# Kernel optimization log

Hardware: AMD Instinct MI355X
Metric: run time of the kernel (lower is better)

## Reference

```python
import jax, jax.numpy as jnp
import numpy as np

N, L, HH, WW, E, NH = 8, 300, 96, 96, 256, 8


def setup_inputs() -> dict:
    key = jax.random.key(0)
    ks = jax.random.split(key, 9)
    return {
        "query_row": jax.random.normal(ks[0], (N, L, E), dtype=jnp.float32),
        "query_col": jax.random.normal(ks[1], (N, L, E), dtype=jnp.float32),
        "key_row": jax.random.normal(ks[2], (N, HH, WW, E), dtype=jnp.float32),
        "key_col": jax.random.normal(ks[3], (N, HH, WW, E), dtype=jnp.float32),
        "value": jax.random.normal(ks[4], (N, HH, WW, E), dtype=jnp.float32),
        "in_proj_weight": jax.random.normal(ks[5], (5 * E, E), dtype=jnp.float32) * 0.02,
        "in_proj_bias": jax.random.normal(ks[6], (5 * E,), dtype=jnp.float32) * 0.02,
        "out_proj_weight": jax.random.normal(ks[7], (E, E), dtype=jnp.float32) * 0.02,
        "out_proj_bias": jax.random.normal(ks[8], (E,), dtype=jnp.float32) * 0.02,
        "num_heads": NH,
    }


def reference(query_row, query_col, key_row, key_col, value,
              in_proj_weight, in_proj_bias, out_proj_weight, out_proj_bias,
              num_heads):
    bsz, tgt_len, embed_dim = query_row.shape
    head_dim = embed_dim // num_heads
    scaling = float(head_dim) ** -0.5

    def proj(x, i):
        w = in_proj_weight[i * embed_dim:(i + 1) * embed_dim]
        b = in_proj_bias[i * embed_dim:(i + 1) * embed_dim]
        return x @ w.T + b

    q_row = proj(query_row, 0) * scaling          # (N, L, E)
    q_col = proj(query_col, 1) * scaling          # (N, L, E)
    k_row = proj(key_row, 2).mean(axis=1)         # mean over H -> (N, W, E)
    k_col = proj(key_col, 3).mean(axis=2)         # mean over W -> (N, H, E)
    v = proj(value, 4)                            # (N, H, W, E)

    heads = lambda t: t.reshape(*t.shape[:-1], num_heads, head_dim)
    qr, qc, kr, kc = heads(q_row), heads(q_col), heads(k_row), heads(k_col)
    vh = heads(v)                                 # (N, H, W, nh, hd)

    # additive row/col decomposed scores -> independent softmaxes
    w_row = jax.nn.softmax(jnp.einsum('blnd,bwnd->bnlw', qr, kr), axis=-1)  # (N,nh,L,W)
    w_col = jax.nn.softmax(jnp.einsum('blnd,bhnd->bnlh', qc, kc), axis=-1)  # (N,nh,L,H)

    # contract col weights with value over H, then row weights over W
    tmp = jnp.einsum('bnlh,bhwnd->bnlwd', w_col, vh)       # (N,nh,L,W,hd)
    out = jnp.einsum('bnlw,bnlwd->blnd', w_row, tmp)       # (N,L,nh,hd)
    out = out.reshape(bsz, tgt_len, embed_dim).transpose(1, 0, 2)  # (L,N,E)
    return out @ out_proj_weight.T + out_proj_bias
```

## Files before the change

kernel.cpp:

```cpp
#include <hip/hip_runtime.h>
#include <cstdint>


typedef __attribute__((ext_vector_type(8))) short short8v;
typedef __attribute__((ext_vector_type(4))) short short4v;
typedef __attribute__((ext_vector_type(4))) float f32x4;

#define SCALE_Q 0.17677669529663687f

#define GLL16(gp, lp)                                                   \
  __builtin_amdgcn_global_load_lds(                                     \
      (const __attribute__((address_space(1))) void*)(gp),              \
      (__attribute__((address_space(3))) void*)(lp), 16, 0, 0)

__device__ __forceinline__ unsigned short f2bf(float x) {
  unsigned int u = __builtin_bit_cast(unsigned int, x);
  u += 0x7FFFu + ((u >> 16) & 1u);
  return (unsigned short)(u >> 16);
}

__device__ __forceinline__ unsigned int cvtpk(float a, float b) {
  unsigned int r;
  asm("v_cvt_pk_bf16_f32 %0, %1, %2" : "=v"(r) : "v"(a), "v"(b));
  return r;
}

__device__ __forceinline__ short8v pack8cvt(const f32x4& lo, const f32x4& hi) {
  union { short8v s; unsigned int u[4]; } z;
  z.u[0] = cvtpk(lo[0], lo[1]);
  z.u[1] = cvtpk(lo[2], lo[3]);
  z.u[2] = cvtpk(hi[0], hi[1]);
  z.u[3] = cvtpk(hi[2], hi[3]);
  return z.s;
}

__device__ __forceinline__ short4v pack4cvt(float a, float b, float c, float d) {
  union { short4v s; unsigned int u[2]; } z;
  z.u[0] = cvtpk(a, b);
  z.u[1] = cvtpk(c, d);
  return z.s;
}

__device__ __forceinline__ short8v pack8(const float4& fa, const float4& fb) {
  short8v v;
  v[0] = (short)f2bf(fa.x); v[1] = (short)f2bf(fa.y);
  v[2] = (short)f2bf(fa.z); v[3] = (short)f2bf(fa.w);
  v[4] = (short)f2bf(fb.x); v[5] = (short)f2bf(fb.y);
  v[6] = (short)f2bf(fb.z); v[7] = (short)f2bf(fb.w);
  return v;
}

__global__ __launch_bounds__(256) void cvt_w_kernel(const float* __restrict__ w_in,
                                                    const float* __restrict__ w_out,
                                                    short* __restrict__ Wb) {
  int idx = blockIdx.x * 256 + threadIdx.x;
  float v = (idx < 327680) ? w_in[idx] : w_out[idx - 327680];
  Wb[idx] = (short)f2bf(v);
}

__global__ __launch_bounds__(512, 4) void mega1_kernel(
    const float* __restrict__ A, const short* __restrict__ Wb,
    const float* __restrict__ bias, short* __restrict__ vvT,
    const float* __restrict__ key_row, const float* __restrict__ key_col,
    float* __restrict__ krm, float* __restrict__ kcm) {
  __shared__ float buf[2][16 * 260];
  __shared__ short Ts[8][32 * 36];
  int blk = blockIdx.x;
  int t = threadIdx.x;

  if ((blk & 1) == 0) {
    int vb_id = blk >> 1;
    int wave = t >> 6, lane = t & 63, r = lane & 15, g = lane >> 4;
    int m0g = vb_id * 96;
    int b_ = vb_id / 96;
    int hw00 = (vb_id - b_ * 96) * 96;
    int chbase = wave * 32;

    short8v bf[8][2];
    {
      const short* wbase = Wb + (size_t)(chbase + r) * 256;
#pragma unroll
      for (int ks = 0; ks < 8; ++ks)
#pragma unroll
        for (int nf = 0; nf < 2; ++nf)
          bf[ks][nf] = *(const short8v*)(wbase + nf * 16 * 256 + ks * 32 + g * 8);
    }
#pragma unroll
    for (int ks = 0; ks < 8; ++ks)
#pragma unroll
      for (int nf = 0; nf < 2; ++nf)
        asm volatile("" : "+a"(bf[ks][nf]));
    float bias_v[2];
#pragma unroll
    for (int nf = 0; nf < 2; ++nf) bias_v[nf] = bias[chbase + nf * 16 + r];

#pragma unroll
    for (int q = 0; q < 2; ++q) {
#pragma unroll
      for (int i = 0; i < 2; ++i) {
        int row = wave * 2 + i;
        const float* gp = A + ((size_t)m0g + q * 16 + row) * 256 + lane * 4;
        GLL16(gp, &buf[q][row * 260]);
      }
    }

    int chg = chbase + (lane & 31);
    int half = lane >> 5;
    short* vbase = vvT + (size_t)(b_ * 8 + (chg >> 5)) * 294912 +
                   (size_t)(chg & 31) * 9216 + hw00;
    const short* tsr = &Ts[wave][(lane & 31) * 36];

#pragma unroll
    for (int tt = 0; tt < 6; ++tt) {
      if (tt == 5)                  asm volatile("s_waitcnt vmcnt(0)" ::: "memory");
      else if (tt == 2 || tt == 4)  asm volatile("s_waitcnt vmcnt(4)" ::: "memory");
      else                          asm volatile("s_waitcnt vmcnt(2)" ::: "memory");
      __builtin_amdgcn_s_barrier();

      f32x4 acc[2] = {};
      const float* bp_ = &buf[tt & 1][0];
#pragma unroll
      for (int ks = 0; ks < 8; ++ks) {
        const float* p = bp_ + r * 260 + ks * 32 + g * 8;
        f32x4 lo = *(const f32x4*)p;
        f32x4 hi = *(const f32x4*)(p + 4);
        short8v af = pack8cvt(lo, hi);
        acc[0] = __builtin_amdgcn_mfma_f32_16x16x32_bf16(af, bf[ks][0], acc[0], 0, 0, 0);
        acc[1] = __builtin_amdgcn_mfma_f32_16x16x32_bf16(af, bf[ks][1], acc[1], 0, 0, 0);
      }

#pragma unroll
      for (int nf = 0; nf < 2; ++nf) {
        float bv = bias_v[nf];
        *(short4v*)&Ts[wave][(nf * 16 + r) * 36 + (tt & 1) * 16 + g * 4] =
            pack4cvt(acc[nf][0] + bv, acc[nf][1] + bv, acc[nf][2] + bv, acc[nf][3] + bv);
      }
      asm volatile("" ::: "memory");

      if (tt & 1) {
        short* gdst = vbase + (tt - 1) * 16 + half * 16;
        const short* src = tsr + half * 16;
        *(short8v*)gdst = *(const short8v*)src;
        *(short8v*)(gdst + 8) = *(const short8v*)(src + 8);
        asm volatile("" ::: "memory");
      }

      __builtin_amdgcn_s_barrier();
      if (tt + 2 < 6) {
#pragma unroll
        for (int i = 0; i < 2; ++i) {
          int row = wave * 2 + i;
          const float* gp = A + ((size_t)m0g + (tt + 2) * 16 + row) * 256 + lane * 4;
          GLL16(gp, &buf[tt & 1][row * 260]);
        }
      }
    }
  } else {
    int id = blk >> 1;
    int sub = t >> 8, u = t & 255;
    int e4 = u & 63, q4 = u >> 6;
    float4* part4 = (float4*)&buf[0][0];
    if (id < 384) {
      int bw = id * 2 + sub;
      int b = bw / 96, w = bw - b * 96;
      const float4* p = (const float4*)(key_row + ((size_t)b * 9216 + w) * 256) +
                        e4 + (size_t)q4 * 24 * 6144;
      float4 s = {0.f, 0.f, 0.f, 0.f};
#pragma unroll
      for (int i = 0; i < 24; ++i) {
        float4 v = p[(size_t)i * 6144];
        s.x += v.x; s.y += v.y; s.z += v.z; s.w += v.w;
      }
      part4[sub * 256 + u] = s;
      __syncthreads();
      if (u < 64) {
        float4 a = part4[sub * 256 + u], c = part4[sub * 256 + u + 64];
        float4 d = part4[sub * 256 + u + 128], e = part4[sub * 256 + u + 192];
        float4 o;
        o.x = (a.x + c.x + d.x + e.x) * (1.f / 96.f);
        o.y = (a.y + c.y + d.y + e.y) * (1.f / 96.f);
        o.z = (a.z + c.z + d.z + e.z) * (1.f / 96.f);
        o.w = (a.w + c.w + d.w + e.w) * (1.f / 96.f);
        ((float4*)krm)[(size_t)bw * 64 + u] = o;
      }
    } else {
      int bh = (id - 384) * 2 + sub;
      const float4* p = (const float4*)(key_col + (size_t)bh * 24576) + e4 +
                        (size_t)q4 * 24 * 64;
      float4 s = {0.f, 0.f, 0.f, 0.f};
#pragma unroll
      for (int i = 0; i < 24; ++i) {
        float4 v = p[(size_t)i * 64];
        s.x += v.x; s.y += v.y; s.z += v.z; s.w += v.w;
      }
      part4[sub * 256 + u] = s;
      __syncthreads();
      if (u < 64) {
        float4 a = part4[sub * 256 + u], c = part4[sub * 256 + u + 64];
        float4 d = part4[sub * 256 + u + 128], e = part4[sub * 256 + u + 192];
        float4 o;
        o.x = (a.x + c.x + d.x + e.x) * (1.f / 96.f);
        o.y = (a.y + c.y + d.y + e.y) * (1.f / 96.f);
        o.z = (a.z + c.z + d.z + e.z) * (1.f / 96.f);
        o.w = (a.w + c.w + d.w + e.w) * (1.f / 96.f);
        ((float4*)kcm)[(size_t)bh * 64 + u] = o;
      }
    }
  }
}

__global__ __launch_bounds__(512) void gemm512(
    const float* __restrict__ krm, const float* __restrict__ kcm,
    const float* __restrict__ qrow, const float* __restrict__ qcol,
    const short* __restrict__ Wb, const float* __restrict__ Bv,
    short* __restrict__ krb, short* __restrict__ kcb,
    short* __restrict__ qrb, short* __restrict__ qcb) {
  __shared__ short As[2][32 * 264];
  int id = blockIdx.x;
  const float* A; short* Cb; const short* Wp; const float* bp; int M, m064;
  float scale;
  if (id < 12)      { A = krm;  Cb = krb; Wp = Wb + 131072; bp = Bv + 512; M = 768;  m064 = id * 64;        scale = 1.f; }
  else if (id < 24) { A = kcm;  Cb = kcb; Wp = Wb + 196608; bp = Bv + 768; M = 768;  m064 = (id - 12) * 64; scale = 1.f; }
  else if (id < 62) { A = qrow; Cb = qrb; Wp = Wb;          bp = Bv;       M = 2400; m064 = (id - 24) * 64; scale = SCALE_Q; }
  else              { A = qcol; Cb = qcb; Wp = Wb + 65536;  bp = Bv + 256; M = 2400; m064 = (id - 62) * 64; scale = SCALE_Q; }

  int t = threadIdx.x, sub = t >> 8, u = t & 255;
  int wave = u >> 6, lane = u & 63, r = lane & 15, g = lane >> 4;
  int m0 = m064 + sub * 32;

  {
    int row = u >> 3, c0 = (u & 7) * 32;
    int mrow = m0 + row; if (mrow >= M) mrow = M - 1;
    const float* ap = A + (size_t)mrow * 256 + c0;
    float4 ld[8];
#pragma unroll
    for (int j = 0; j < 8; ++j) ld[j] = *(const float4*)(ap + j * 4);
    short* dst = &As[sub][row * 264 + c0];
#pragma unroll
    for (int j = 0; j < 4; ++j)
      *(short8v*)(dst + j * 8) = pack8(ld[2 * j], ld[2 * j + 1]);
  }
  __syncthreads();

  f32x4 acc[2][4] = {};
  const short* wbase = Wp + (size_t)(wave * 64 + r) * 256;
#pragma unroll
  for (int ks = 0; ks < 8; ++ks) {
    short8v af0 = *(const short8v*)&As[sub][r * 264 + ks * 32 + g * 8];
    short8v af1 = *(const short8v*)&As[sub][(16 + r) * 264 + ks * 32 + g * 8];
    short8v bf[4];
#pragma unroll
    for (int nf = 0; nf < 4; ++nf)
      bf[nf] = *(const short8v*)(wbase + nf * 16 * 256 + ks * 32 + g * 8);
#pragma unroll
    for (int nf = 0; nf < 4; ++nf) {
      acc[0][nf] = __builtin_amdgcn_mfma_f32_16x16x32_bf16(af0, bf[nf], acc[0][nf], 0, 0, 0);
      acc[1][nf] = __builtin_amdgcn_mfma_f32_16x16x32_bf16(af1, bf[nf], acc[1][nf], 0, 0, 0);
    }
  }

#pragma unroll
  for (int mf = 0; mf < 2; ++mf)
#pragma unroll
    for (int nf = 0; nf < 4; ++nf) {
      int nn = wave * 64 + nf * 16 + r;
      float bval = bp[nn];
#pragma unroll
      for (int i = 0; i < 4; ++i) {
        int m = m0 + mf * 16 + g * 4 + i;
        if (m >= M) continue;
        Cb[(size_t)m * 256 + nn] = (short)f2bf((acc[mf][nf][i] + bval) * scale);
      }
    }
}

__global__ __launch_bounds__(512) void gemm512_out(
    const float* __restrict__ A0, const float* __restrict__ Aadd,
    const short* __restrict__ Wp, const float* __restrict__ bp,
    float* __restrict__ Cf) {
  __shared__ short As[2][32 * 264];
  const int M = 2400;
  int t = threadIdx.x, sub = t >> 8, u = t & 255;
  int wave = u >> 6, lane = u & 63, r = lane & 15, g = lane >> 4;
  int m0 = blockIdx.x * 64 + sub * 32;

  {
    int row = u >> 3, c0 = (u & 7) * 32;
    int mrow = m0 + row; if (mrow >= M) mrow = M - 1;
    size_t off = (size_t)mrow * 256 + c0;
    const float* ap = A0 + off;
    const float* aq = Aadd + off;
    float4 ld[8];
#pragma unroll
    for (int j = 0; j < 8; ++j) {
      float4 x = *(const float4*)(ap + j * 4);
      float4 e = *(const float4*)(aq + j * 4);
      x.x += e.x; x.y += e.y; x.z += e.z; x.w += e.w;
      ld[j] = x;
    }
    short* dst = &As[sub][row * 264 + c0];
#pragma unroll
    for (int j = 0; j < 4; ++j)
      *(short8v*)(dst + j * 8) = pack8(ld[2 * j], ld[2 * j + 1]);
  }
  __syncthreads();

  f32x4 acc[2][4] = {};
  const short* wbase = Wp + (size_t)(wave * 64 + r) * 256;
#pragma unroll
  for (int ks = 0; ks < 8; ++ks) {
    short8v af0 = *(const short8v*)&As[sub][r * 264 + ks * 32 + g * 8];
    short8v af1 = *(const short8v*)&As[sub][(16 + r) * 264 + ks * 32 + g * 8];
    short8v bf[4];
#pragma unroll
    for (int nf = 0; nf < 4; ++nf)
      bf[nf] = *(const short8v*)(wbase + nf * 16 * 256 + ks * 32 + g * 8);
#pragma unroll
    for (int nf = 0; nf < 4; ++nf) {
      acc[0][nf] = __builtin_amdgcn_mfma_f32_16x16x32_bf16(af0, bf[nf], acc[0][nf], 0, 0, 0);
      acc[1][nf] = __builtin_amdgcn_mfma_f32_16x16x32_bf16(af1, bf[nf], acc[1][nf], 0, 0, 0);
    }
  }

#pragma unroll
  for (int mf = 0; mf < 2; ++mf)
#pragma unroll
    for (int nf = 0; nf < 4; ++nf) {
      int nn = wave * 64 + nf * 16 + r;
      float bval = bp[nn];
#pragma unroll
      for (int i = 0; i < 4; ++i) {
        int m = m0 + mf * 16 + g * 4 + i;
        if (m >= M) continue;
        int bb = m / 300, ll = m - bb * 300;
        Cf[((size_t)ll * 8 + bb) * 256 + nn] = acc[mf][nf][i] + bval;
      }
    }
}

__global__ __launch_bounds__(64) void scores_softmax_v2(
    const short* __restrict__ qrb, const short* __restrict__ qcb,
    const short* __restrict__ krb, const short* __restrict__ kcb,
    short* __restrict__ wrowB, float* __restrict__ wcolT) {
  int lchunk = blockIdx.x, bn = blockIdx.y, kind = blockIdx.z;
  int b = bn >> 3, n = bn & 7;
  int lane = threadIdx.x;
  int r = lane & 15, g = lane >> 4;
  const short* qb = kind ? qcb : qrb;
  const short* kb = kind ? kcb : krb;
  int l0 = lchunk * 80;

  short8v a[5], bfr[6];
#pragma unroll
  for (int lf = 0; lf < 5; ++lf) {
    int l = l0 + lf * 16 + r;
    if (l > 299) l = 299;
    a[lf] = *(const short8v*)(qb + ((size_t)b * 300 + l) * 256 + n * 32 + g * 8);
  }
#pragma unroll
  for (int f = 0; f < 6; ++f)
    bfr[f] = *(const short8v*)(kb + ((size_t)b * 96 + f * 16 + r) * 256 + n * 32 + g * 8);

  f32x4 c[5][6];
#pragma unroll
  for (int lf = 0; lf < 5; ++lf)
#pragma unroll
    for (int f = 0; f < 6; ++f) {
      f32x4 z = {};
      c[lf][f] = __builtin_amdgcn_mfma_f32_16x16x32_bf16(a[lf], bfr[f], z, 0, 0, 0);
    }

#pragma unroll
  for (int lf = 0; lf < 5; ++lf)
#pragma unroll
    for (int i = 0; i < 4; ++i) {
      float m = c[lf][0][i];
#pragma unroll
      for (int f = 1; f < 6; ++f) m = fmaxf(m, c[lf][f][i]);
#pragma unroll
      for (int mask = 1; mask <= 8; mask <<= 1) m = fmaxf(m, __shfl_xor(m, mask, 64));
      float e[6], s = 0.f;
#pragma unroll
      for (int f = 0; f < 6; ++f) { e[f] = __expf(c[lf][f][i] - m); s += e[f]; }
#pragma unroll
      for (int mask = 1; mask <= 8; mask <<= 1) s += __shfl_xor(s, mask, 64);
      float inv = 1.f / s;
#pragma unroll
      for (int f = 0; f < 6; ++f) c[lf][f][i] = e[f] * inv;
    }

  if (kind == 0) {
#pragma unroll
    for (int lf = 0; lf < 5; ++lf)
#pragma unroll
      for (int i = 0; i < 4; ++i) {
        int l = l0 + lf * 16 + g * 4 + i;
        bool ok = (l < 300);
#pragma unroll
        for (int f = 0; f < 6; ++f) {
          float wv = ok ? c[lf][f][i] : 0.f;
          wrowB[((size_t)bn * 320 + l) * 96 + f * 16 + r] = (short)f2bf(wv);
        }
      }
  } else {
#pragma unroll
    for (int lf = 0; lf < 5; ++lf)
#pragma unroll
      for (int f = 0; f < 6; ++f) {
        int l = l0 + lf * 16 + g * 4;
        f32x4 wv = c[lf][f];
#pragma unroll
        for (int i = 0; i < 4; ++i) if (l + i >= 300) wv[i] = 0.f;
        *(f32x4*)(wcolT + ((size_t)bn * 96 + f * 16 + r) * 320 + l) = wv;
      }
  }
}

__global__ __launch_bounds__(512, 2) void attn_kernel(
    const short* __restrict__ wrowB, const float* __restrict__ wcolT,
    const short* __restrict__ vvT, float* __restrict__ part0,
    float* __restrict__ part1) {
  __shared__ f32x4 cmb[3][2][4][64];
  int i = blockIdx.x;
  int xcd = i & 7, j = i >> 3;
  int grp = j / 10, rem = j - grp * 10;
  int bn = grp * 8 + xcd;
  int lh = rem >> 1, hh2 = rem & 1;
  int b = bn >> 3, n = bn & 7;
  int t = threadIdx.x, wave = t >> 6, lane = t & 63;
  int df = wave & 1, hq = wave >> 1;
  int lbase = lh * 64;
  int r = lane & 15, g = lane >> 4;
  int hbase = hh2 * 48 + hq * 12;

  short8v a[4][3];
  const short* wr = wrowB + (size_t)bn * 320 * 96;
#pragma unroll
  for (int lf = 0; lf < 4; ++lf)
#pragma unroll
    for (int ks = 0; ks < 3; ++ks)
      a[lf][ks] = *(const short8v*)(wr + (lbase + lf * 16 + r) * 96 + ks * 32 + g * 8);

  const short* vb = vvT + (size_t)bn * 294912 + (size_t)(df * 16 + r) * 9216 + hbase * 96;
  const float* wcb = wcolT + ((size_t)bn * 96 + hbase) * 320 + lbase + g * 4;

  f32x4 acc[4] = {};
  short8v b0[3], b1[3];
  f32x4 w0[4], w1[4];
#pragma unroll
  for (int ks = 0; ks < 3; ++ks) b0[ks] = *(const short8v*)(vb + ks * 32 + g * 8);
#pragma unroll
  for (int lf = 0; lf < 4; ++lf) w0[lf] = *(const f32x4*)(wcb + lf * 16);

#pragma unroll
  for (int h2 = 0; h2 < 6; ++h2) {
    int h = h2 * 2;
#pragma unroll
    for (int ks = 0; ks < 3; ++ks) b1[ks] = *(const short8v*)(vb + (h + 1) * 96 + ks * 32 + g * 8);
#pragma unroll
    for (int lf = 0; lf < 4; ++lf) w1[lf] = *(const f32x4*)(wcb + (h + 1) * 320 + lf * 16);
    {
      f32x4 R[4] = {};
#pragma unroll
      for (int ks = 0; ks < 3; ++ks)
#pragma unroll
        for (int lf = 0; lf < 4; ++lf)
          R[lf] = __builtin_amdgcn_mfma_f32_16x16x32_bf16(a[lf][ks], b0[ks], R[lf], 0, 0, 0);
#pragma unroll
      for (int lf = 0; lf < 4; ++lf) acc[lf] += w0[lf] * R[lf];
    }
    if (h2 < 5) {
#pragma unroll
      for (int ks = 0; ks < 3; ++ks) b0[ks] = *(const short8v*)(vb + (h + 2) * 96 + ks * 32 + g * 8);
#pragma unroll
      for (int lf = 0; lf < 4; ++lf) w0[lf] = *(const f32x4*)(wcb + (h + 2) * 320 + lf * 16);
    }
    {
      f32x4 R[4] = {};
#pragma unroll
      for (int ks = 0; ks < 3; ++ks)
#pragma unroll
        for (int lf = 0; lf < 4; ++lf)
          R[lf] = __builtin_amdgcn_mfma_f32_16x16x32_bf16(a[lf][ks], b1[ks], R[lf], 0, 0, 0);
#pragma unroll
      for (int lf = 0; lf < 4; ++lf) acc[lf] += w1[lf] * R[lf];
    }
  }

  if (hq > 0) {
#pragma unroll
    for (int lf = 0; lf < 4; ++lf) cmb[hq - 1][df][lf][lane] = acc[lf];
  }
  __syncthreads();
  if (hq == 0) {
    float* po = hh2 ? part1 : part0;
#pragma unroll
    for (int lf = 0; lf < 4; ++lf) {
      f32x4 o = acc[lf];
#pragma unroll
      for (int q = 0; q < 3; ++q) o += cmb[q][df][lf][lane];
#pragma unroll
      for (int i2 = 0; i2 < 4; ++i2) {
        int l = lbase + lf * 16 + g * 4 + i2;
        if (l < 300)
          po[((size_t)b * 300 + l) * 256 + n * 32 + df * 16 + r] = o[i2];
      }
    }
  }
}

extern "C" void kernel_launch(void* const* d_in, const int* in_sizes, int n_in,
                              void* d_out, int out_size, void* d_ws, size_t ws_size,
                              hipStream_t stream) {
  const float* query_row = (const float*)d_in[0];
  const float* query_col = (const float*)d_in[1];
  const float* key_row   = (const float*)d_in[2];
  const float* key_col   = (const float*)d_in[3];
  const float* value     = (const float*)d_in[4];
  const float* W         = (const float*)d_in[5];
  const float* Bv        = (const float*)d_in[6];
  const float* Wout      = (const float*)d_in[7];
  const float* Bout      = (const float*)d_in[8];

  float* ws = (float*)d_ws;
  float* krm   = ws;
  float* kcm   = krm + 196608;
  float* part0 = kcm + 196608;
  float* part1 = part0 + 614400;
  float* wcolT = part1 + 614400;
  short* qrb   = (short*)(wcolT + 1966080);
  short* qcb   = qrb + 614400;
  short* krb   = qcb + 614400;
  short* kcb   = krb + 196608;
  short* wrowB = kcb + 196608;
  short* vvT   = wrowB + 1966080;
  short* Wb    = vvT + 18874368;

  cvt_w_kernel<<<1536, 256, 0, stream>>>(W, Wout, Wb);
  mega1_kernel<<<1536, 512, 0, stream>>>(value, Wb + 262144, Bv + 1024, vvT,
                                         key_row, key_col, krm, kcm);
  gemm512<<<100, 512, 0, stream>>>(krm, kcm, query_row, query_col, Wb, Bv,
                                   krb, kcb, qrb, qcb);
  scores_softmax_v2<<<dim3(4, 64, 2), 64, 0, stream>>>(qrb, qcb, krb, kcb, wrowB, wcolT);
  attn_kernel<<<640, 512, 0, stream>>>(wrowB, wcolT, vvT, part0, part1);
  gemm512_out<<<38, 512, 0, stream>>>(part0, part1, Wb + 327680, Bout, (float*)d_out);
}
```

Before: 155.4 us.

## Restructure attention to stage V in LDS and fuse mean-pool into value projection blocks

The attention kernel is rewritten to use 256 blocks, each covering a quarter of H for one batch-head. V slices are double-buffered in swizzled LDS through global_load_lds, the column weights are staged once in LDS, and each wave handles 80 rows of L. The output partials go to four buffers that the output GEMM now sums. The value-projection kernel no longer interleaves separate mean-pool blocks; every block projects value and then does one key mean-pool chunk, which halves the grid. This trades more LDS use and fewer blocks (less parallelism) for reuse of V across waves, and it adds extra partial traffic.

Measured after the change: 306.1 us. +97.0%, slower.

```diff
diff --git a/kernel.cpp b/kernel.cpp
--- a/kernel.cpp
+++ b/kernel.cpp
@@ -58,153 +58,149 @@
   Wb[idx] = (short)f2bf(v);
 }
 
-__global__ __launch_bounds__(512, 4) void mega1_kernel(
+__global__ __launch_bounds__(512, 4) void vpm_kernel(
     const float* __restrict__ A, const short* __restrict__ Wb,
     const float* __restrict__ bias, short* __restrict__ vvT,
     const float* __restrict__ key_row, const float* __restrict__ key_col,
     float* __restrict__ krm, float* __restrict__ kcm) {
   __shared__ float buf[2][16 * 260];
   __shared__ short Ts[8][32 * 36];
-  int blk = blockIdx.x;
   int t = threadIdx.x;
-
-  if ((blk & 1) == 0) {
-    int vb_id = blk >> 1;
-    int wave = t >> 6, lane = t & 63, r = lane & 15, g = lane >> 4;
-    int m0g = vb_id * 96;
-    int b_ = vb_id / 96;
-    int hw00 = (vb_id - b_ * 96) * 96;
-    int chbase = wave * 32;
-
-    short8v bf[8][2];
-    {
-      const short* wbase = Wb + (size_t)(chbase + r) * 256;
-#pragma unroll
-      for (int ks = 0; ks < 8; ++ks)
-#pragma unroll
-        for (int nf = 0; nf < 2; ++nf)
-          bf[ks][nf] = *(const short8v*)(wbase + nf * 16 * 256 + ks * 32 + g * 8);
-    }
+  int wave = t >> 6, lane = t & 63, r = lane & 15, g = lane >> 4;
+  int m0g = blockIdx.x * 96;
+  int b_ = blockIdx.x / 96;
+  int hw00 = (blockIdx.x - b_ * 96) * 96;
+  int chbase = wave * 32;
+
+  short8v bf[8][2];
+  {
+    const short* wbase = Wb + (size_t)(chbase + r) * 256;
 #pragma unroll
     for (int ks = 0; ks < 8; ++ks)
 #pragma unroll
       for (int nf = 0; nf < 2; ++nf)
-        asm volatile("" : "+a"(bf[ks][nf]));
-    float bias_v[2];
-#pragma unroll
-    for (int nf = 0; nf < 2; ++nf) bias_v[nf] = bias[chbase + nf * 16 + r];
-
-#pragma unroll
-    for (int q = 0; q < 2; ++q) {
+        bf[ks][nf] = *(const short8v*)(wbase + nf * 16 * 256 + ks * 32 + g * 8);
+  }
+#pragma unroll
+  for (int ks = 0; ks < 8; ++ks)
+#pragma unroll
+    for (int nf = 0; nf < 2; ++nf)
+      asm volatile("" : "+a"(bf[ks][nf]));
+  float bias_v[2];
+#pragma unroll
+  for (int nf = 0; nf < 2; ++nf) bias_v[nf] = bias[chbase + nf * 16 + r];
+
+#pragma unroll
+  for (int q = 0; q < 2; ++q) {
+#pragma unroll
+    for (int i = 0; i < 2; ++i) {
+      int row = wave * 2 + i;
+      const float* gp = A + ((size_t)m0g + q * 16 + row) * 256 + lane * 4;
+      GLL16(gp, &buf[q][row * 260]);
+    }
+  }
+
+  int chg = chbase + (lane & 31);
+  int half = lane >> 5;
+  short* vbase = vvT + (size_t)(b_ * 8 + (chg >> 5)) * 294912 +
+                 (size_t)(chg & 31) * 9216 + hw00;
+  const short* tsr = &Ts[wave][(lane & 31) * 36];
+
+#pragma unroll
+  for (int tt = 0; tt < 6; ++tt) {
+    if (tt == 5)                  asm volatile("s_waitcnt vmcnt(0)" ::: "memory");
+    else if (tt == 2 || tt == 4)  asm volatile("s_waitcnt vmcnt(4)" ::: "memory");
+    else                          asm volatile("s_waitcnt vmcnt(2)" ::: "memory");
+    __builtin_amdgcn_s_barrier();
+
+    f32x4 acc[2] = {};
+    const float* bp_ = &buf[tt & 1][0];
+#pragma unroll
+    for (int ks = 0; ks < 8; ++ks) {
+      const float* p = bp_ + r * 260 + ks * 32 + g * 8;
+      f32x4 lo = *(const f32x4*)p;
+      f32x4 hi = *(const f32x4*)(p + 4);
+      short8v af = pack8cvt(lo, hi);
+      acc[0] = __builtin_amdgcn_mfma_f32_16x16x32_bf16(af, bf[ks][0], acc[0], 0, 0, 0);
+      acc[1] = __builtin_amdgcn_mfma_f32_16x16x32_bf16(af, bf[ks][1], acc[1], 0, 0, 0);
+    }
+
+#pragma unroll
+    for (int nf = 0; nf < 2; ++nf) {
+      float bv = bias_v[nf];
+      *(short4v*)&Ts[wave][(nf * 16 + r) * 36 + (tt & 1) * 16 + g * 4] =
+          pack4cvt(acc[nf][0] + bv, acc[nf][1] + bv, acc[nf][2] + bv, acc[nf][3] + bv);
+    }
+    asm volatile("" ::: "memory");
+
+    if (tt & 1) {
+      short* gdst = vbase + (tt - 1) * 16 + half * 16;
+      const short* src = tsr + half * 16;
+      *(short8v*)gdst = *(const short8v*)src;
+      *(short8v*)(gdst + 8) = *(const short8v*)(src + 8);
+      asm volatile("" ::: "memory");
+    }
+
+    __builtin_amdgcn_s_barrier();
+    if (tt + 2 < 6) {
 #pragma unroll
       for (int i = 0; i < 2; ++i) {
         int row = wave * 2 + i;
-        const float* gp = A + ((size_t)m0g + q * 16 + row) * 256 + lane * 4;
-        GLL16(gp, &buf[q][row * 260]);
+        const float* gp = A + ((size_t)m0g + (tt + 2) * 16 + row) * 256 + lane * 4;
+        GLL16(gp, &buf[tt & 1][row * 260]);
       }
     }
-
-    int chg = chbase + (lane & 31);
-    int half = lane >> 5;
-    short* vbase = vvT + (size_t)(b_ * 8 + (chg >> 5)) * 294912 +
-                   (size_t)(chg & 31) * 9216 + hw00;
-    const short* tsr = &Ts[wave][(lane & 31) * 36];
-
-#pragma unroll
-    for (int tt = 0; tt < 6; ++tt) {
-      if (tt == 5)                  asm volatile("s_waitcnt vmcnt(0)" ::: "memory");
-      else if (tt == 2 || tt == 4)  asm volatile("s_waitcnt vmcnt(4)" ::: "memory");
-      else                          asm volatile("s_waitcnt vmcnt(2)" ::: "memory");
-      __builtin_amdgcn_s_barrier();
-
-      f32x4 acc[2] = {};
-      const float* bp_ = &buf[tt & 1][0];
-#pragma unroll
-      for (int ks = 0; ks < 8; ++ks) {
-        const float* p = bp_ + r * 260 + ks * 32 + g * 8;
-        f32x4 lo = *(const f32x4*)p;
-        f32x4 hi = *(const f32x4*)(p + 4);
-        short8v af = pack8cvt(lo, hi);
-        acc[0] = __builtin_amdgcn_mfma_f32_16x16x32_bf16(af, bf[ks][0], acc[0], 0, 0, 0);
-        acc[1] = __builtin_amdgcn_mfma_f32_16x16x32_bf16(af, bf[ks][1], acc[1], 0, 0, 0);
-      }
-
-#pragma unroll
-      for (int nf = 0; nf < 2; ++nf) {
-        float bv = bias_v[nf];
-        *(short4v*)&Ts[wave][(nf * 16 + r) * 36 + (tt & 1) * 16 + g * 4] =
-            pack4cvt(acc[nf][0] + bv, acc[nf][1] + bv, acc[nf][2] + bv, acc[nf][3] + bv);
-      }
-      asm volatile("" ::: "memory");
-
-      if (tt & 1) {
-        short* gdst = vbase + (tt - 1) * 16 + half * 16;
-        const short* src = tsr + half * 16;
-        *(short8v*)gdst = *(const short8v*)src;
-        *(short8v*)(gdst + 8) = *(const short8v*)(src + 8);
-        asm volatile("" ::: "memory");
-      }
-
-      __builtin_amdgcn_s_barrier();
-      if (tt + 2 < 6) {
-#pragma unroll
-        for (int i = 0; i < 2; ++i) {
-          int row = wave * 2 + i;
-          const float* gp = A + ((size_t)m0g + (tt + 2) * 16 + row) * 256 + lane * 4;
-          GLL16(gp, &buf[tt & 1][row * 260]);
-        }
-      }
+  }
+
+  __syncthreads();
+  int id = blockIdx.x;
+  int sub = t >> 8, u = t & 255;
+  int e4 = u & 63, q4 = u >> 6;
+  float4* part4 = (float4*)&buf[0][0];
+  if (id < 384) {
+    int bw = id * 2 + sub;
+    int b = bw / 96, w = bw - b * 96;
+    const float4* p = (const float4*)(key_row + ((size_t)b * 9216 + w) * 256) +
+                      e4 + (size_t)q4 * 24 * 6144;
+    float4 s = {0.f, 0.f, 0.f, 0.f};
+#pragma unroll
+    for (int i = 0; i < 24; ++i) {
+      float4 v = p[(size_t)i * 6144];
+      s.x += v.x; s.y += v.y; s.z += v.z; s.w += v.w;
+    }
+    part4[sub * 256 + u] = s;
+    __syncthreads();
+    if (u < 64) {
+      float4 a = part4[sub * 256 + u], c = part4[sub * 256 + u + 64];
+      float4 d = part4[sub * 256 + u + 128], e = part4[sub * 256 + u + 192];
+      float4 o;
+      o.x = (a.x + c.x + d.x + e.x) * (1.f / 96.f);
+      o.y = (a.y + c.y + d.y + e.y) * (1.f / 96.f);
+      o.z = (a.z + c.z + d.z + e.z) * (1.f / 96.f);
+      o.w = (a.w + c.w + d.w + e.w) * (1.f / 96.f);
+      ((float4*)krm)[(size_t)bw * 64 + u] = o;
     }
   } else {
-    int id = blk >> 1;
-    int sub = t >> 8, u = t & 255;
-    int e4 = u & 63, q4 = u >> 6;
-    float4* part4 = (float4*)&buf[0][0];
-    if (id < 384) {
-      int bw = id * 2 + sub;
-      int b = bw / 96, w = bw - b * 96;
-      const float4* p = (const float4*)(key_row + ((size_t)b * 9216 + w) * 256) +
-                        e4 + (size_t)q4 * 24 * 6144;
-      float4 s = {0.f, 0.f, 0.f, 0.f};
-#pragma unroll
-      for (int i = 0; i < 24; ++i) {
-        float4 v = p[(size_t)i * 6144];
-        s.x += v.x; s.y += v.y; s.z += v.z; s.w += v.w;
-      }
-      part4[sub * 256 + u] = s;
-      __syncthreads();
-      if (u < 64) {
-        float4 a = part4[sub * 256 + u], c = part4[sub * 256 + u + 64];
-        float4 d = part4[sub * 256 + u + 128], e = part4[sub * 256 + u + 192];
-        float4 o;
-        o.x = (a.x + c.x + d.x + e.x) * (1.f / 96.f);
-        o.y = (a.y + c.y + d.y + e.y) * (1.f / 96.f);
-        o.z = (a.z + c.z + d.z + e.z) * (1.f / 96.f);
-        o.w = (a.w + c.w + d.w + e.w) * (1.f / 96.f);
-        ((float4*)krm)[(size_t)bw * 64 + u] = o;
-      }
-    } else {
-      int bh = (id - 384) * 2 + sub;
-      const float4* p = (const float4*)(key_col + (size_t)bh * 24576) + e4 +
-                        (size_t)q4 * 24 * 64;
-      float4 s = {0.f, 0.f, 0.f, 0.f};
-#pragma unroll
-      for (int i = 0; i < 24; ++i) {
-        float4 v = p[(size_t)i * 64];
-        s.x += v.x; s.y += v.y; s.z += v.z; s.w += v.w;
-      }
-      part4[sub * 256 + u] = s;
-      __syncthreads();
-      if (u < 64) {
-        float4 a = part4[sub * 256 + u], c = part4[sub * 256 + u + 64];
-        float4 d = part4[sub * 256 + u + 128], e = part4[sub * 256 + u + 192];
-        float4 o;
-        o.x = (a.x + c.x + d.x + e.x) * (1.f / 96.f);
-        o.y = (a.y + c.y + d.y + e.y) * (1.f / 96.f);
-        o.z = (a.z + c.z + d.z + e.z) * (1.f / 96.f);
-        o.w = (a.w + c.w + d.w + e.w) * (1.f / 96.f);
-        ((float4*)kcm)[(size_t)bh * 64 + u] = o;
-      }
+    int bh = (id - 384) * 2 + sub;
+    const float4* p = (const float4*)(key_col + (size_t)bh * 24576) + e4 +
+                      (size_t)q4 * 24 * 64;
+    float4 s = {0.f, 0.f, 0.f, 0.f};
+#pragma unroll
+    for (int i = 0; i < 24; ++i) {
+      float4 v = p[(size_t)i * 64];
+      s.x += v.x; s.y += v.y; s.z += v.z; s.w += v.w;
+    }
+    part4[sub * 256 + u] = s;
+    __syncthreads();
+    if (u < 64) {
+      float4 a = part4[sub * 256 + u], c = part4[sub * 256 + u + 64];
+      float4 d = part4[sub * 256 + u + 128], e = part4[sub * 256 + u + 192];
+      float4 o;
+      o.x = (a.x + c.x + d.x + e.x) * (1.f / 96.f);
+      o.y = (a.y + c.y + d.y + e.y) * (1.f / 96.f);
+      o.z = (a.z + c.z + d.z + e.z) * (1.f / 96.f);
+      o.w = (a.w + c.w + d.w + e.w) * (1.f / 96.f);
+      ((float4*)kcm)[(size_t)bh * 64 + u] = o;
     }
   }
 }
@@ -248,14 +244,14 @@
   for (int ks = 0; ks < 8; ++ks) {
     short8v af0 = *(const short8v*)&As[sub][r * 264 + ks * 32 + g * 8];
     short8v af1 = *(const short8v*)&As[sub][(16 + r) * 264 + ks * 32 + g * 8];
-    short8v bf[4];
+    short8v bfr[4];
 #pragma unroll
     for (int nf = 0; nf < 4; ++nf)
-      bf[nf] = *(const short8v*)(wbase + nf * 16 * 256 + ks * 32 + g * 8);
+      bfr[nf] = *(const short8v*)(wbase + nf * 16 * 256 + ks * 32 + g * 8);
 #pragma unroll
     for (int nf = 0; nf < 4; ++nf) {
-      acc[0][nf] = __builtin_amdgcn_mfma_f32_16x16x32_bf16(af0, bf[nf], acc[0][nf], 0, 0, 0);
-      acc[1][nf] = __builtin_amdgcn_mfma_f32_16x16x32_bf16(af1, bf[nf], acc[1][nf], 0, 0, 0);
+      acc[0][nf] = __builtin_amdgcn_mfma_f32_16x16x32_bf16(af0, bfr[nf], acc[0][nf], 0, 0, 0);
+      acc[1][nf] = __builtin_amdgcn_mfma_f32_16x16x32_bf16(af1, bfr[nf], acc[1][nf], 0, 0, 0);
     }
   }
 
@@ -275,7 +271,8 @@
 }
 
 __global__ __launch_bounds__(512) void gemm512_out(
-    const float* __restrict__ A0, const float* __restrict__ Aadd,
+    const float* __restrict__ p0, const float* __restrict__ p1,
+    const float* __restrict__ p2, const float* __restrict__ p3,
     const short* __restrict__ Wp, const float* __restrict__ bp,
     float* __restrict__ Cf) {
   __shared__ short As[2][32 * 264];
@@ -288,14 +285,15 @@
     int row = u >> 3, c0 = (u & 7) * 32;
     int mrow = m0 + row; if (mrow >= M) mrow = M - 1;
     size_t off = (size_t)mrow * 256 + c0;
-    const float* ap = A0 + off;
-    const float* aq = Aadd + off;
     float4 ld[8];
 #pragma unroll
     for (int j = 0; j < 8; ++j) {
-      float4 x = *(const float4*)(ap + j * 4);
-      float4 e = *(const float4*)(aq + j * 4);
-      x.x += e.x; x.y += e.y; x.z += e.z; x.w += e.w;
+      float4 x = *(const float4*)(p0 + off + j * 4);
+      float4 y = *(const float4*)(p1 + off + j * 4);
+      float4 z = *(const float4*)(p2 + off + j * 4);
+      float4 w = *(const float4*)(p3 + off + j * 4);
+      x.x += y.x + z.x + w.x; x.y += y.y + z.y + w.y;
+      x.z += y.z + z.z + w.z; x.w += y.w + z.w + w.w;
       ld[j] = x;
     }
     short* dst = &As[sub][row * 264 + c0];
@@ -311,14 +309,14 @@
   for (int ks = 0; ks < 8; ++ks) {
     short8v af0 = *(const short8v*)&As[sub][r * 264 + ks * 32 + g * 8];
     short8v af1 = *(const short8v*)&As[sub][(16 + r) * 264 + ks * 32 + g * 8];
-    short8v bf[4];
+    short8v bfr[4];
 #pragma unroll
     for (int nf = 0; nf < 4; ++nf)
-      bf[nf] = *(const short8v*)(wbase + nf * 16 * 256 + ks * 32 + g * 8);
+      bfr[nf] = *(const short8v*)(wbase + nf * 16 * 256 + ks * 32 + g * 8);
 #pragma unroll
     for (int nf = 0; nf < 4; ++nf) {
-      acc[0][nf] = __builtin_amdgcn_mfma_f32_16x16x32_bf16(af0, bf[nf], acc[0][nf], 0, 0, 0);
-      acc[1][nf] = __builtin_amdgcn_mfma_f32_16x16x32_bf16(af1, bf[nf], acc[1][nf], 0, 0, 0);
+      acc[0][nf] = __builtin_amdgcn_mfma_f32_16x16x32_bf16(af0, bfr[nf], acc[0][nf], 0, 0, 0);
+      acc[1][nf] = __builtin_amdgcn_mfma_f32_16x16x32_bf16(af1, bfr[nf], acc[1][nf], 0, 0, 0);
     }
   }
 
@@ -416,97 +414,97 @@
   }
 }
 
-__global__ __launch_bounds__(512, 2) void attn_kernel(
+__global__ __launch_bounds__(512, 2) void attn_v4(
     const short* __restrict__ wrowB, const float* __restrict__ wcolT,
-    const short* __restrict__ vvT, float* __restrict__ part0,
-    float* __restrict__ part1) {
-  __shared__ f32x4 cmb[3][2][4][64];
-  int i = blockIdx.x;
-  int xcd = i & 7, j = i >> 3;
-  int grp = j / 10, rem = j - grp * 10;
-  int bn = grp * 8 + xcd;
-  int lh = rem >> 1, hh2 = rem & 1;
+    const short* __restrict__ vvT, float* __restrict__ part) {
+  __shared__ short Vs[2][384 * 8];
+  __shared__ float wcs[24 * 320];
+  int bid = blockIdx.x;
+  int xcd = bid & 7, idx = bid >> 3;
+  int hq = idx & 3, bn = (idx >> 2) * 8 + xcd;
+  int hbase = hq * 24;
   int b = bn >> 3, n = bn & 7;
   int t = threadIdx.x, wave = t >> 6, lane = t & 63;
-  int df = wave & 1, hq = wave >> 1;
-  int lbase = lh * 64;
+  int df = wave & 1, lq = wave >> 1;
+  int l0 = lq * 80;
   int r = lane & 15, g = lane >> 4;
-  int hbase = hh2 * 48 + hq * 12;
-
-  short8v a[4][3];
+
+  const short* vbn = vvT + (size_t)bn * 294912;
+
+  if (wave < 6) {
+    int gg = wave * 64 + lane;
+    int d = gg / 12, q = gg - d * 12;
+    int qs = q ^ (d & 3);
+    const short* s0 = vbn + (size_t)d * 9216 + (hbase + 0) * 96 + qs * 8;
+    GLL16(s0, &Vs[0][gg * 8]);
+    const short* s1 = vbn + (size_t)d * 9216 + (hbase + 1) * 96 + qs * 8;
+    GLL16(s1, &Vs[1][gg * 8]);
+  } else {
+    const float* wcsrc = wcolT + ((size_t)bn * 96 + hbase) * 320;
+    int c0 = (wave - 6) * 64 + lane;
+#pragma unroll
+    for (int k = 0; k < 15; ++k) {
+      int c = c0 + k * 128;
+      GLL16(wcsrc + c * 4, &wcs[c * 4]);
+    }
+  }
+
+  short8v a[5][3];
   const short* wr = wrowB + (size_t)bn * 320 * 96;
 #pragma unroll
-  for (int lf = 0; lf < 4; ++lf)
+  for (int lf = 0; lf < 5; ++lf)
 #pragma unroll
     for (int ks = 0; ks < 3; ++ks)
-      a[lf][ks] = *(const short8v*)(wr + (lbase + lf * 16 + r) * 96 + ks * 32 + g * 8);
-
-  const short* vb = vvT + (size_t)bn * 294912 + (size_t)(df * 16 + r) * 9216 + hbase * 96;
-  const float* wcb = wcolT + ((size_t)bn * 96 + hbase) * 320 + lbase + g * 4;
-
-  f32x4 acc[4] = {};
-  short8v b0[3], b1[3];
-  f32x4 w0[4], w1[4];
-#pragma unroll
-  for (int ks = 0; ks < 3; ++ks) b0[ks] = *(const short8v*)(vb + ks * 32 + g * 8);
-#pragma unroll
-  for (int lf = 0; lf < 4; ++lf) w0[lf] = *(const f32x4*)(wcb + lf * 16);
-
-#pragma unroll
-  for (int h2 = 0; h2 < 6; ++h2) {
-    int h = h2 * 2;
-#pragma unroll
-    for (int ks = 0; ks < 3; ++ks) b1[ks] = *(const short8v*)(vb + (h + 1) * 96 + ks * 32 + g * 8);
-#pragma unroll
-    for (int lf = 0; lf < 4; ++lf) w1[lf] = *(const f32x4*)(wcb + (h + 1) * 320 + lf * 16);
-    {
-      f32x4 R[4] = {};
-#pragma unroll
-      for (int ks = 0; ks < 3; ++ks)
-#pragma unroll
-        for (int lf = 0; lf < 4; ++lf)
-          R[lf] = __builtin_amdgcn_mfma_f32_16x16x32_bf16(a[lf][ks], b0[ks], R[lf], 0, 0, 0);
-#pragma unroll
-      for (int lf = 0; lf < 4; ++lf) acc[lf] += w0[lf] * R[lf];
-    }
-    if (h2 < 5) {
-#pragma unroll
-      for (int ks = 0; ks < 3; ++ks) b0[ks] = *(const short8v*)(vb + (h + 2) * 96 + ks * 32 + g * 8);
-#pragma unroll
-      for (int lf = 0; lf < 4; ++lf) w0[lf] = *(const f32x4*)(wcb + (h + 2) * 320 + lf * 16);
-    }
-    {
-      f32x4 R[4] = {};
-#pragma unroll
-      for (int ks = 0; ks < 3; ++ks)
-#pragma unroll
-        for (int lf = 0; lf < 4; ++lf)
-          R[lf] = __builtin_amdgcn_mfma_f32_16x16x32_bf16(a[lf][ks], b1[ks], R[lf], 0, 0, 0);
-#pragma unroll
-      for (int lf = 0; lf < 4; ++lf) acc[lf] += w1[lf] * R[lf];
-    }
-  }
-
-  if (hq > 0) {
-#pragma unroll
-    for (int lf = 0; lf < 4; ++lf) cmb[hq - 1][df][lf][lane] = acc[lf];
-  }
-  __syncthreads();
-  if (hq == 0) {
-    float* po = hh2 ? part1 : part0;
-#pragma unroll
-    for (int lf = 0; lf < 4; ++lf) {
-      f32x4 o = acc[lf];
-#pragma unroll
-      for (int q = 0; q < 3; ++q) o += cmb[q][df][lf][lane];
-#pragma unroll
-      for (int i2 = 0; i2 < 4; ++i2) {
-        int l = lbase + lf * 16 + g * 4 + i2;
-        if (l < 300)
-          po[((size_t)b * 300 + l) * 256 + n * 32 + df * 16 + r] = o[i2];
-      }
-    }
-  }
+      a[lf][ks] = *(const short8v*)(wr + (l0 + lf * 16 + r) * 96 + ks * 32 + g * 8);
+
+  f32x4 acc[5] = {};
+  int d = df * 16 + r;
+  int sw = d & 3;
+
+#pragma unroll
+  for (int hs = 0; hs < 24; ++hs) {
+    if (hs < 23) asm volatile("s_waitcnt vmcnt(1)" ::: "memory");
+    else         asm volatile("s_waitcnt vmcnt(0)" ::: "memory");
+    __builtin_amdgcn_s_barrier();
+
+    const short* vsb = &Vs[hs & 1][0];
+    short8v bfr[3];
+#pragma unroll
+    for (int ks = 0; ks < 3; ++ks) {
+      int q = ks * 4 + g;
+      bfr[ks] = *(const short8v*)(vsb + ((size_t)d * 12 + (q ^ sw)) * 8);
+    }
+    f32x4 R[5] = {};
+#pragma unroll
+    for (int ks = 0; ks < 3; ++ks)
+#pragma unroll
+      for (int lf = 0; lf < 5; ++lf)
+        R[lf] = __builtin_amdgcn_mfma_f32_16x16x32_bf16(a[lf][ks], bfr[ks], R[lf], 0, 0, 0);
+#pragma unroll
+    for (int lf = 0; lf < 5; ++lf) {
+      f32x4 w = *(const f32x4*)&wcs[hs * 320 + l0 + lf * 16 + g * 4];
+      acc[lf] += w * R[lf];
+    }
+
+    __builtin_amdgcn_s_barrier();
+    if (hs + 2 < 24 && wave < 6) {
+      int gg = wave * 64 + lane;
+      int d2 = gg / 12, q2 = gg - d2 * 12;
+      int qs2 = q2 ^ (d2 & 3);
+      const short* src = vbn + (size_t)d2 * 9216 + (hbase + hs + 2) * 96 + qs2 * 8;
+      GLL16(src, &Vs[hs & 1][gg * 8]);
+    }
+  }
+
+  float* po = part + (size_t)hq * 614400 + (size_t)b * 300 * 256 + n * 32 + d;
+#pragma unroll
+  for (int lf = 0; lf < 5; ++lf)
+#pragma unroll
+    for (int i2 = 0; i2 < 4; ++i2) {
+      int l = l0 + lf * 16 + g * 4 + i2;
+      if (l < 300) po[(size_t)l * 256] = acc[lf][i2];
+      po += 0;
+    }
 }
 
 extern "C" void kernel_launch(void* const* d_in, const int* in_sizes, int n_in,
@@ -525,9 +523,8 @@
   float* ws = (float*)d_ws;
   float* krm   = ws;
   float* kcm   = krm + 196608;
-  float* part0 = kcm + 196608;
-  float* part1 = part0 + 614400;
-  float* wcolT = part1 + 614400;
+  float* part  = kcm + 196608;
+  float* wcolT = part + 2457600;
   short* qrb   = (short*)(wcolT + 1966080);
   short* qcb   = qrb + 614400;
   short* krb   = qcb + 614400;
@@ -537,11 +534,13 @@
   short* Wb    = vvT + 18874368;
 
   cvt_w_kernel<<<1536, 256, 0, stream>>>(W, Wout, Wb);
-  mega1_kernel<<<1536, 512, 0, stream>>>(value, Wb + 262144, Bv + 1024, vvT,
-                                         key_row, key_col, krm, kcm);
+  vpm_kernel<<<768, 512, 0, stream>>>(value, Wb + 262144, Bv + 1024, vvT,
+                                      key_row, key_col, krm, kcm);
   gemm512<<<100, 512, 0, stream>>>(krm, kcm, query_row, query_col, Wb, Bv,
                                    krb, kcb, qrb, qcb);
   scores_softmax_v2<<<dim3(4, 64, 2), 64, 0, stream>>>(qrb, qcb, krb, kcb, wrowB, wcolT);
-  attn_kernel<<<640, 512, 0, stream>>>(wrowB, wcolT, vvT, part0, part1);
-  gemm512_out<<<38, 512, 0, stream>>>(part0, part1, Wb + 327680, Bout, (float*)d_out);
-}
+  attn_v4<<<256, 512, 0, stream>>>(wrowB, wcolT, vvT, part);
+  gemm512_out<<<38, 512, 0, stream>>>(part, part + 614400, part + 1228800,
+                                      part + 1843200, Wb + 327680, Bout,
+                                      (float*)d_out);
+}
```
